# Kernel tuning notes

Hardware: AMD Instinct MI355X
Metric: run time of the kernel (lower is better)

Reference implementation:

```python
import math
import jax, jax.numpy as jnp
import numpy as np

B, S, E = 4, 2048, 1024

def setup_inputs() -> dict:
    key = jax.random.key(0)
    k1, k2, k3 = jax.random.split(key, 3)
    X = jax.random.normal(k1, (B, S, E), dtype=jnp.float32)
    # nn.Linear(E, 3E): weight [3E, E], bias [3E]; scale weights for sane softmax
    W = jax.random.normal(k2, (3 * E, E), dtype=jnp.float32) * (1.0 / math.sqrt(E))
    b = jax.random.normal(k3, (3 * E,), dtype=jnp.float32) * 0.01
    return {"X": X, "W": W, "b": b}

def reference(X, W, b):
    E_ = X.shape[-1]
    # fused QKV projection: X @ W^T + b -> [B, S, 3E]
    qkv = jnp.einsum('bse,fe->bsf', X, W) + b
    q, k, v = jnp.split(qkv, 3, axis=-1)
    scores = jnp.einsum('bqe,bke->bqk', q, k) / math.sqrt(E_)
    attention_weight = jax.nn.softmax(scores, axis=-1)  # [B, S, S]
    output = jnp.einsum('bqk,bke->bqe', attention_weight, v)
    return (output, attention_weight)
```

## Files before the change

### kernel.cpp

```cpp
#include <hip/hip_runtime.h>
#include <math.h>

typedef __bf16 bf16;
typedef __bf16 bf16x4 __attribute__((ext_vector_type(4)));
typedef __bf16 bf16x8 __attribute__((ext_vector_type(8)));
typedef float f32x4 __attribute__((ext_vector_type(4)));

#define MODE_QKV    0
#define MODE_SCORES 1
#define MODE_PV     2

__device__ inline void gload_lds16(const bf16* g, bf16* l) {
    __builtin_amdgcn_global_load_lds(
        (const __attribute__((address_space(1))) void*)g,
        (__attribute__((address_space(3))) void*)l, 16, 0, 0);
}

#define DSR(dst, base, imm)                                                 \
    asm volatile("ds_read_b128 %0, %1 offset:%2"                            \
        : "=v"(dst)                                                         \
        : "v"((const __attribute__((address_space(3))) bf16*)(base)),       \
          "i"(imm))

#define MF(i, j) acc[i][j] = __builtin_amdgcn_mfma_f32_16x16x32_bf16(       \
    af[i], bq[j], acc[i][j], 0, 0, 0);

template <int MODE, int NT>
__global__ __launch_bounds__(256, 2) void mfma_nt(
    const bf16* __restrict__ A, const bf16* __restrict__ B,
    const float* __restrict__ bias, void* __restrict__ Cv,
    int lda, int ldb, int ldc,
    long sA, long sB, long sC, float alpha)
{
    A += (long)blockIdx.z * sA;
    B += (long)blockIdx.z * sB;

    __shared__ bf16 As[3 * 8192] __attribute__((aligned(16)));
    __shared__ bf16 Bs[3 * 4096] __attribute__((aligned(16)));

    const int t  = threadIdx.x;
    const int m0 = blockIdx.y * 256;
    const int n0 = blockIdx.x * 128;

    const int lane = t & 63;
    const int wave = t >> 6;
    const int wr   = (wave >> 1) * 128;
    const int wc   = (wave & 1) * 64;
    const int fr   = lane & 15;
    const int kq8  = lane >> 4;

    const bf16* gA0; const bf16* gA1; const bf16* gA2; const bf16* gA3;
    const bf16* gB0; const bf16* gB1;
    {
        const int c0 = t,        r0 = c0 >> 2, h0 = ((c0 & 3) ^ ((r0 >> 1) & 3)) * 8;
        const int c1 = t + 256,  r1 = c1 >> 2, h1 = ((c1 & 3) ^ ((r1 >> 1) & 3)) * 8;
        const int c2 = t + 512,  r2 = c2 >> 2, h2 = ((c2 & 3) ^ ((r2 >> 1) & 3)) * 8;
        const int c3 = t + 768,  r3 = c3 >> 2, h3 = ((c3 & 3) ^ ((r3 >> 1) & 3)) * 8;
        gA0 = A + (long)(m0 + r0) * lda + h0;
        gA1 = A + (long)(m0 + r1) * lda + h1;
        gA2 = A + (long)(m0 + r2) * lda + h2;
        gA3 = A + (long)(m0 + r3) * lda + h3;
        gB0 = B + (long)(n0 + r0) * ldb + h0;
        gB1 = B + (long)(n0 + r1) * ldb + h1;
    }

    const int swz = kq8 ^ ((fr >> 1) & 3);
    const bf16* pA = As + (wr + fr) * 32 + swz * 8;
    const bf16* pB = Bs + (wc + fr) * 32 + swz * 8;

    f32x4 acc[8][4] = {};
    bf16x8 af[8], bq[4];
    int kofs = 64;

#define STAGE6(SS, ko)                                                      \
    gload_lds16(gA0 + (ko), &As[(SS) * 8192 + t * 8]);                      \
    gload_lds16(gA1 + (ko), &As[(SS) * 8192 + (t + 256) * 8]);              \
    gload_lds16(gA2 + (ko), &As[(SS) * 8192 + (t + 512) * 8]);              \
    gload_lds16(gA3 + (ko), &As[(SS) * 8192 + (t + 768) * 8]);              \
    gload_lds16(gB0 + (ko), &Bs[(SS) * 4096 + t * 8]);                      \
    gload_lds16(gB1 + (ko), &Bs[(SS) * 4096 + (t + 256) * 8]);

#define TB(CS, STG) do {                                                    \
    if constexpr ((STG) == 1) {                                             \
        constexpr int SS = ((CS) + 2) % 3;                                  \
        STAGE6(SS, kofs);                                                   \
        kofs += 32;                                                         \
    }                                                                       \
    DSR(af[0], pA, (CS) * 16384 + 0);                                       \
    DSR(af[1], pA, (CS) * 16384 + 1024);                                    \
    DSR(af[2], pA, (CS) * 16384 + 2048);                                    \
    DSR(af[3], pA, (CS) * 16384 + 3072);                                    \
    DSR(bq[0], pB, (CS) * 8192 + 0);                                        \
    DSR(bq[1], pB, (CS) * 8192 + 1024);                                     \
    DSR(bq[2], pB, (CS) * 8192 + 2048);                                     \
    DSR(bq[3], pB, (CS) * 8192 + 3072);                                     \
    DSR(af[4], pA, (CS) * 16384 + 4096);                                    \
    DSR(af[5], pA, (CS) * 16384 + 5120);                                    \
    DSR(af[6], pA, (CS) * 16384 + 6144);                                    \
    DSR(af[7], pA, (CS) * 16384 + 7168);                                    \
    asm volatile("s_waitcnt lgkmcnt(6)" ::: "memory");                      \
    __builtin_amdgcn_sched_barrier(0);                                      \
    __builtin_amdgcn_s_setprio(1);                                          \
    MF(0,0) MF(0,1) MF(1,0) MF(1,1) MF(2,0) MF(2,1) MF(3,0) MF(3,1)         \
    asm volatile("s_waitcnt lgkmcnt(4)" ::: "memory");                      \
    __builtin_amdgcn_sched_barrier(0);                                      \
    MF(0,2) MF(0,3) MF(1,2) MF(1,3) MF(2,2) MF(2,3) MF(3,2) MF(3,3)         \
    asm volatile("s_waitcnt lgkmcnt(0)" ::: "memory");                      \
    __builtin_amdgcn_sched_barrier(0);                                      \
    MF(4,0) MF(4,1) MF(5,0) MF(5,1) MF(6,0) MF(6,1) MF(7,0) MF(7,1)         \
    MF(4,2) MF(4,3) MF(5,2) MF(5,3) MF(6,2) MF(6,3) MF(7,2) MF(7,3)         \
    __builtin_amdgcn_s_setprio(0);                                          \
    if constexpr ((STG) == 1)                                               \
        asm volatile("s_waitcnt vmcnt(6)" ::: "memory");                    \
    else if constexpr ((STG) == 0)                                          \
        asm volatile("s_waitcnt vmcnt(0)" ::: "memory");                    \
    if constexpr ((STG) != 2) __builtin_amdgcn_s_barrier();                 \
} while (0)

    STAGE6(0, 0);
    STAGE6(1, 32);
    asm volatile("s_waitcnt vmcnt(6)" ::: "memory");
    __builtin_amdgcn_s_barrier();

    static_assert(NT % 3 != 0, "peel pattern assumes NT%3 in {1,2}");
    if constexpr (NT % 3 == 2) {
        TB(0, 1); TB(1, 1);
        for (int g = 0; g < (NT - 5) / 3; ++g) { TB(2, 1); TB(0, 1); TB(1, 1); }
        TB(2, 1); TB(0, 0); TB(1, 2);
    } else {
        TB(0, 1);
        for (int g = 0; g < (NT - 4) / 3; ++g) { TB(1, 1); TB(2, 1); TB(0, 1); }
        TB(1, 1); TB(2, 0); TB(0, 2);
    }
#undef TB
#undef STAGE6

    const int r4 = (lane >> 4) * 4;
    if constexpr (MODE == MODE_PV) {
        float* C = (float*)Cv + (long)blockIdx.z * sC;
#pragma unroll
        for (int j = 0; j < 4; j++) {
            const int col = n0 + wc + j * 16 + fr;
#pragma unroll
            for (int i = 0; i < 8; i++)
#pragma unroll
                for (int r = 0; r < 4; r++) {
                    const long row = m0 + wr + i * 16 + r4 + r;
                    C[row * ldc + col] = acc[i][j][r];
                }
        }
    } else {
        bf16* C = (bf16*)Cv + (long)blockIdx.z * sC;
#pragma unroll
        for (int j = 0; j < 4; j++) {
            const int col = n0 + wc + j * 16 + fr;
            const float bv = (MODE == MODE_QKV) ? bias[col] : 0.f;
#pragma unroll
            for (int i = 0; i < 8; i++)
#pragma unroll
                for (int r = 0; r < 4; r++) {
                    const long row = m0 + wr + i * 16 + r4 + r;
                    float v = acc[i][j][r];
                    if constexpr (MODE == MODE_QKV)
                        C[row * ldc + col] = (bf16)(v + bv);
                    else
                        C[row * ldc + col] = (bf16)__expf(alpha * v);
                }
        }
    }
}

__global__ __launch_bounds__(256) void f32_to_bf16(
    const float* __restrict__ in, bf16* __restrict__ out, long n)
{
    long i = ((long)blockIdx.x * 256 + threadIdx.x) * 4;
    if (i < n) {
        float4 v = *(const float4*)(in + i);
        bf16x4 o = { (bf16)v.x, (bf16)v.y, (bf16)v.z, (bf16)v.w };
        *(bf16x4*)(out + i) = o;
    }
}

__global__ __launch_bounds__(256) void transpose_v(
    const bf16* __restrict__ V, bf16* __restrict__ Vt)
{
    __shared__ bf16 tile[32][33];
    const bf16* Vb  = V  + (long)blockIdx.z * 2048 * 3072;
    bf16*       Vtb = Vt + (long)blockIdx.z * 1024 * 2048;
    const int s0 = blockIdx.x * 32, e0 = blockIdx.y * 32;
    const int tx = threadIdx.x & 31, ty = threadIdx.x >> 5;
#pragma unroll
    for (int i = 0; i < 32; i += 8)
        tile[ty + i][tx] = Vb[(long)(s0 + ty + i) * 3072 + e0 + tx];
    __syncthreads();
#pragma unroll
    for (int i = 0; i < 32; i += 8)
        Vtb[(long)(e0 + ty + i) * 2048 + s0 + tx] = tile[tx][ty + i];
}

__global__ __launch_bounds__(256) void norm_rows(
    bf16* __restrict__ Pu, float* __restrict__ out1)
{
    bf16* p  = Pu   + (long)blockIdx.x * 2048;
    float* o = out1 + (long)blockIdx.x * 2048;
    const int t = threadIdx.x;
    bf16x8 v = *(const bf16x8*)(p + t * 8);
    float f[8];
    float s = 0.f;
#pragma unroll
    for (int k = 0; k < 8; k++) { f[k] = (float)v[k]; s += f[k]; }
#pragma unroll
    for (int off = 32; off > 0; off >>= 1) s += __shfl_xor(s, off);
    __shared__ float red[4];
    const int wid = t >> 6, lane = t & 63;
    if (lane == 0) red[wid] = s;
    __syncthreads();
    s = red[0] + red[1] + red[2] + red[3];
    const float inv = 1.0f / s;
    float4 a, b;
    a.x = f[0] * inv; a.y = f[1] * inv; a.z = f[2] * inv; a.w = f[3] * inv;
    b.x = f[4] * inv; b.y = f[5] * inv; b.z = f[6] * inv; b.w = f[7] * inv;
    *(float4*)(o + t * 8)     = a;
    *(float4*)(o + t * 8 + 4) = b;
    bf16x8 w;
#pragma unroll
    for (int k = 0; k < 8; k++) w[k] = (bf16)(f[k] * inv);
    *(bf16x8*)(p + t * 8) = w;
}

extern "C" void kernel_launch(void* const* d_in, const int* in_sizes, int n_in,
                              void* d_out, int out_size, void* d_ws, size_t ws_size,
                              hipStream_t stream)
{
    const int B = 4, S = 2048, E = 1024;
    const float* X    = (const float*)d_in[0];
    const float* W    = (const float*)d_in[1];
    const float* bias = (const float*)d_in[2];

    float* out0 = (float*)d_out;
    float* out1 = out0 + (long)B * S * E;

    char* ws = (char*)d_ws;
    bf16* qkvb = (bf16*)(ws);
    bf16* Vt   = (bf16*)(ws + 50331648);
    bf16* Pu   = (bf16*)(ws + 67108864);
    bf16* Xb   = (bf16*)(ws + 67108864);
    bf16* Wb   = (bf16*)(ws + 83886080);

    f32_to_bf16<<<(long)B * S * E / 1024, 256, 0, stream>>>(X, Xb, (long)B * S * E);
    f32_to_bf16<<<(long)3 * E * E / 1024, 256, 0, stream>>>(W, Wb, (long)3 * E * E);

    mfma_nt<MODE_QKV, 32><<<dim3(3 * E / 128, B * S / 256, 1), 256, 0, stream>>>(
        Xb, Wb, bias, qkvb, E, E, 3 * E, 0, 0, 0, 1.0f);

    transpose_v<<<dim3(S / 32, E / 32, B), 256, 0, stream>>>(qkvb + 2 * E, Vt);

    mfma_nt<MODE_SCORES, 32><<<dim3(S / 128, S / 256, B), 256, 0, stream>>>(
        qkvb, qkvb + E, nullptr, Pu, 3 * E, 3 * E, S,
        (long)S * 3 * E, (long)S * 3 * E, (long)S * S, 0.03125f);

    norm_rows<<<B * S, 256, 0, stream>>>(Pu, out1);

    mfma_nt<MODE_PV, 64><<<dim3(E / 128, S / 256, B), 256, 0, stream>>>(
        Pu, Vt, nullptr, out0, S, S, E,
        (long)S * S, (long)E * S, (long)S * E, 1.0f);
}
```

Measured before the change: 304.1 us.

## Split-K the PV GEMM with atomics and use a 2-slot LDS ring for QKV

The PV GEMM is split into two K halves across blockIdx.z, doubling the grid. Partial results are accumulated into a zeroed output via atomic float adds, which needs a memset first. Separately, the QKV projection switches to a 2-stage LDS ring with full vmcnt waits, freeing shared memory at the cost of less load/compute overlap. The PV grid was only 128 blocks, so the split aims to fill more CUs, but it adds atomic traffic and an extra memset pass over the output.

```diff
diff --git a/kernel.cpp b/kernel.cpp
--- a/kernel.cpp
+++ b/kernel.cpp
@@ -25,18 +25,23 @@
 #define MF(i, j) acc[i][j] = __builtin_amdgcn_mfma_f32_16x16x32_bf16(       \
     af[i], bq[j], acc[i][j], 0, 0, 0);
 
-template <int MODE, int NT>
+template <int MODE, int NT, int RING>
 __global__ __launch_bounds__(256, 2) void mfma_nt(
     const bf16* __restrict__ A, const bf16* __restrict__ B,
     const float* __restrict__ bias, void* __restrict__ Cv,
     int lda, int ldb, int ldc,
     long sA, long sB, long sC, float alpha)
 {
-    A += (long)blockIdx.z * sA;
-    B += (long)blockIdx.z * sB;
-
-    __shared__ bf16 As[3 * 8192] __attribute__((aligned(16)));
-    __shared__ bf16 Bs[3 * 4096] __attribute__((aligned(16)));
+    constexpr bool SPLIT = (MODE == MODE_PV);
+
+    const int bz    = blockIdx.z;
+    const int batch = SPLIT ? (bz >> 1) : bz;
+    const int koff  = SPLIT ? (bz & 1) * (NT * 32) : 0;
+    A += (long)batch * sA + koff;
+    B += (long)batch * sB + koff;
+
+    __shared__ bf16 As[RING * 8192] __attribute__((aligned(16)));
+    __shared__ bf16 Bs[RING * 4096] __attribute__((aligned(16)));
 
     const int t  = threadIdx.x;
     const int m0 = blockIdx.y * 256;
@@ -70,7 +75,7 @@
 
     f32x4 acc[8][4] = {};
     bf16x8 af[8], bq[4];
-    int kofs = 64;
+    int kofs;
 
 #define STAGE6(SS, ko)                                                      \
     gload_lds16(gA0 + (ko), &As[(SS) * 8192 + t * 8]);                      \
@@ -82,7 +87,7 @@
 
 #define TB(CS, STG) do {                                                    \
     if constexpr ((STG) == 1) {                                             \
-        constexpr int SS = ((CS) + 2) % 3;                                  \
+        constexpr int SS = ((CS) + RING - 1) % RING;                        \
         STAGE6(SS, kofs);                                                   \
         kofs += 32;                                                         \
     }                                                                       \
@@ -110,34 +115,49 @@
     MF(4,0) MF(4,1) MF(5,0) MF(5,1) MF(6,0) MF(6,1) MF(7,0) MF(7,1)         \
     MF(4,2) MF(4,3) MF(5,2) MF(5,3) MF(6,2) MF(6,3) MF(7,2) MF(7,3)         \
     __builtin_amdgcn_s_setprio(0);                                          \
-    if constexpr ((STG) == 1)                                               \
-        asm volatile("s_waitcnt vmcnt(6)" ::: "memory");                    \
-    else if constexpr ((STG) == 0)                                          \
+    if constexpr ((STG) == 1) {                                             \
+        if constexpr (RING == 3)                                            \
+            asm volatile("s_waitcnt vmcnt(6)" ::: "memory");                \
+        else                                                                \
+            asm volatile("s_waitcnt vmcnt(0)" ::: "memory");                \
+    } else if constexpr ((STG) == 0)                                        \
         asm volatile("s_waitcnt vmcnt(0)" ::: "memory");                    \
     if constexpr ((STG) != 2) __builtin_amdgcn_s_barrier();                 \
 } while (0)
 
-    STAGE6(0, 0);
-    STAGE6(1, 32);
-    asm volatile("s_waitcnt vmcnt(6)" ::: "memory");
-    __builtin_amdgcn_s_barrier();
-
-    static_assert(NT % 3 != 0, "peel pattern assumes NT%3 in {1,2}");
-    if constexpr (NT % 3 == 2) {
-        TB(0, 1); TB(1, 1);
-        for (int g = 0; g < (NT - 5) / 3; ++g) { TB(2, 1); TB(0, 1); TB(1, 1); }
-        TB(2, 1); TB(0, 0); TB(1, 2);
+    if constexpr (RING == 3) {
+        STAGE6(0, 0);
+        STAGE6(1, 32);
+        kofs = 64;
+        asm volatile("s_waitcnt vmcnt(6)" ::: "memory");
+        __builtin_amdgcn_s_barrier();
+
+        static_assert(NT % 3 != 0, "peel pattern assumes NT%3 in {1,2}");
+        if constexpr (NT % 3 == 2) {
+            TB(0, 1); TB(1, 1);
+            for (int g = 0; g < (NT - 5) / 3; ++g) { TB(2, 1); TB(0, 1); TB(1, 1); }
+            TB(2, 1); TB(0, 0); TB(1, 2);
+        } else {
+            TB(0, 1);
+            for (int g = 0; g < (NT - 4) / 3; ++g) { TB(1, 1); TB(2, 1); TB(0, 1); }
+            TB(1, 1); TB(2, 0); TB(0, 2);
+        }
     } else {
-        TB(0, 1);
-        for (int g = 0; g < (NT - 4) / 3; ++g) { TB(1, 1); TB(2, 1); TB(0, 1); }
-        TB(1, 1); TB(2, 0); TB(0, 2);
+        STAGE6(0, 0);
+        kofs = 32;
+        asm volatile("s_waitcnt vmcnt(0)" ::: "memory");
+        __builtin_amdgcn_s_barrier();
+
+        static_assert(NT % 2 == 0, "2-slot peel assumes even NT");
+        for (int g = 0; g < NT / 2 - 1; ++g) { TB(0, 1); TB(1, 1); }
+        TB(0, 1); TB(1, 2);
     }
 #undef TB
 #undef STAGE6
 
     const int r4 = (lane >> 4) * 4;
     if constexpr (MODE == MODE_PV) {
-        float* C = (float*)Cv + (long)blockIdx.z * sC;
+        float* C = (float*)Cv + (long)batch * sC;
 #pragma unroll
         for (int j = 0; j < 4; j++) {
             const int col = n0 + wc + j * 16 + fr;
@@ -146,11 +166,11 @@
 #pragma unroll
                 for (int r = 0; r < 4; r++) {
                     const long row = m0 + wr + i * 16 + r4 + r;
-                    C[row * ldc + col] = acc[i][j][r];
+                    unsafeAtomicAdd(&C[row * ldc + col], acc[i][j][r]);
                 }
         }
     } else {
-        bf16* C = (bf16*)Cv + (long)blockIdx.z * sC;
+        bf16* C = (bf16*)Cv + (long)batch * sC;
 #pragma unroll
         for (int j = 0; j < 4; j++) {
             const int col = n0 + wc + j * 16 + fr;
@@ -250,18 +270,19 @@
     f32_to_bf16<<<(long)B * S * E / 1024, 256, 0, stream>>>(X, Xb, (long)B * S * E);
     f32_to_bf16<<<(long)3 * E * E / 1024, 256, 0, stream>>>(W, Wb, (long)3 * E * E);
 
-    mfma_nt<MODE_QKV, 32><<<dim3(3 * E / 128, B * S / 256, 1), 256, 0, stream>>>(
+    mfma_nt<MODE_QKV, 32, 2><<<dim3(3 * E / 128, B * S / 256, 1), 256, 0, stream>>>(
         Xb, Wb, bias, qkvb, E, E, 3 * E, 0, 0, 0, 1.0f);
 
     transpose_v<<<dim3(S / 32, E / 32, B), 256, 0, stream>>>(qkvb + 2 * E, Vt);
 
-    mfma_nt<MODE_SCORES, 32><<<dim3(S / 128, S / 256, B), 256, 0, stream>>>(
+    mfma_nt<MODE_SCORES, 32, 3><<<dim3(S / 128, S / 256, B), 256, 0, stream>>>(
         qkvb, qkvb + E, nullptr, Pu, 3 * E, 3 * E, S,
         (long)S * 3 * E, (long)S * 3 * E, (long)S * S, 0.03125f);
 
     norm_rows<<<B * S, 256, 0, stream>>>(Pu, out1);
 
-    mfma_nt<MODE_PV, 64><<<dim3(E / 128, S / 256, B), 256, 0, stream>>>(
+    hipMemsetAsync(out0, 0, (size_t)B * S * E * sizeof(float), stream);
+    mfma_nt<MODE_PV, 32, 3><<<dim3(E / 128, S / 256, 2 * B), 256, 0, stream>>>(
         Pu, Vt, nullptr, out0, S, S, E,
         (long)S * S, (long)E * S, (long)S * E, 1.0f);
 }
```

New measurement: 359.7 us. 1.18x slower.

## Prefetch next K-tile's A/B fragments from LDS during second MFMA half

Applied to the files above, without the earlier changes.

Restructures the GEMM main loop so the lower A fragments and all B fragments for the next K-step are read from LDS right after the barrier, while the upper-half MFMAs of the current step run. Fragments are double-buffered in registers, and the global-to-LDS stage is issued mid-iteration. The loop peel is rewritten for NT of 32 or 64 only. This aims to hide LDS read latency behind MFMA work, at the cost of more VGPRs under launch_bounds(256,2), which risks spills or lower occupancy.

```diff
diff --git a/kernel.cpp b/kernel.cpp
--- a/kernel.cpp
+++ b/kernel.cpp
@@ -21,9 +21,6 @@
         : "=v"(dst)                                                         \
         : "v"((const __attribute__((address_space(3))) bf16*)(base)),       \
           "i"(imm))
-
-#define MF(i, j) acc[i][j] = __builtin_amdgcn_mfma_f32_16x16x32_bf16(       \
-    af[i], bq[j], acc[i][j], 0, 0, 0);
 
 template <int MODE, int NT>
 __global__ __launch_bounds__(256, 2) void mfma_nt(
@@ -69,8 +66,10 @@
     const bf16* pB = Bs + (wc + fr) * 32 + swz * 8;
 
     f32x4 acc[8][4] = {};
-    bf16x8 af[8], bq[4];
-    int kofs = 64;
+    bf16x8 afhi[4];
+    bf16x8 alo[2][4];
+    bf16x8 bqq[2][4];
+    int kofs;
 
 #define STAGE6(SS, ko)                                                      \
     gload_lds16(gA0 + (ko), &As[(SS) * 8192 + t * 8]);                      \
@@ -80,60 +79,84 @@
     gload_lds16(gB0 + (ko), &Bs[(SS) * 4096 + t * 8]);                      \
     gload_lds16(gB1 + (ko), &Bs[(SS) * 4096 + (t + 256) * 8]);
 
-#define TB(CS, STG) do {                                                    \
-    if constexpr ((STG) == 1) {                                             \
-        constexpr int SS = ((CS) + 2) % 3;                                  \
-        STAGE6(SS, kofs);                                                   \
-        kofs += 32;                                                         \
-    }                                                                       \
-    DSR(af[0], pA, (CS) * 16384 + 0);                                       \
-    DSR(af[1], pA, (CS) * 16384 + 1024);                                    \
-    DSR(af[2], pA, (CS) * 16384 + 2048);                                    \
-    DSR(af[3], pA, (CS) * 16384 + 3072);                                    \
-    DSR(bq[0], pB, (CS) * 8192 + 0);                                        \
-    DSR(bq[1], pB, (CS) * 8192 + 1024);                                     \
-    DSR(bq[2], pB, (CS) * 8192 + 2048);                                     \
-    DSR(bq[3], pB, (CS) * 8192 + 3072);                                     \
-    DSR(af[4], pA, (CS) * 16384 + 4096);                                    \
-    DSR(af[5], pA, (CS) * 16384 + 5120);                                    \
-    DSR(af[6], pA, (CS) * 16384 + 6144);                                    \
-    DSR(af[7], pA, (CS) * 16384 + 7168);                                    \
-    asm volatile("s_waitcnt lgkmcnt(6)" ::: "memory");                      \
+#define MFU(i, j, P) acc[i][j] = __builtin_amdgcn_mfma_f32_16x16x32_bf16(   \
+    alo[P][i], bqq[P][j], acc[i][j], 0, 0, 0);
+#define MFL(i, j, P) acc[4 + i][j] = __builtin_amdgcn_mfma_f32_16x16x32_bf16(\
+    afhi[i], bqq[P][j], acc[4 + i][j], 0, 0, 0);
+
+#define TBP(C, P, STG) do {                                                 \
+    DSR(afhi[0], pA, (C) * 16384 + 4096);                                   \
+    DSR(afhi[1], pA, (C) * 16384 + 5120);                                   \
+    DSR(afhi[2], pA, (C) * 16384 + 6144);                                   \
+    DSR(afhi[3], pA, (C) * 16384 + 7168);                                   \
+    asm volatile("s_waitcnt lgkmcnt(4)" ::: "memory");                      \
     __builtin_amdgcn_sched_barrier(0);                                      \
     __builtin_amdgcn_s_setprio(1);                                          \
-    MF(0,0) MF(0,1) MF(1,0) MF(1,1) MF(2,0) MF(2,1) MF(3,0) MF(3,1)         \
-    asm volatile("s_waitcnt lgkmcnt(4)" ::: "memory");                      \
-    __builtin_amdgcn_sched_barrier(0);                                      \
-    MF(0,2) MF(0,3) MF(1,2) MF(1,3) MF(2,2) MF(2,3) MF(3,2) MF(3,3)         \
+    MFU(0,0,P) MFU(0,1,P) MFU(1,0,P) MFU(1,1,P)                             \
+    MFU(2,0,P) MFU(2,1,P) MFU(3,0,P) MFU(3,1,P)                             \
+    MFU(0,2,P) MFU(0,3,P) MFU(1,2,P) MFU(1,3,P)                             \
+    MFU(2,2,P) MFU(2,3,P) MFU(3,2,P) MFU(3,3,P)                             \
+    __builtin_amdgcn_s_setprio(0);                                          \
+    if constexpr ((STG) == 1) { STAGE6(((C) + 2) % 3, kofs); kofs += 32; }  \
     asm volatile("s_waitcnt lgkmcnt(0)" ::: "memory");                      \
     __builtin_amdgcn_sched_barrier(0);                                      \
-    MF(4,0) MF(4,1) MF(5,0) MF(5,1) MF(6,0) MF(6,1) MF(7,0) MF(7,1)         \
-    MF(4,2) MF(4,3) MF(5,2) MF(5,3) MF(6,2) MF(6,3) MF(7,2) MF(7,3)         \
-    __builtin_amdgcn_s_setprio(0);                                          \
     if constexpr ((STG) == 1)                                               \
         asm volatile("s_waitcnt vmcnt(6)" ::: "memory");                    \
     else if constexpr ((STG) == 0)                                          \
         asm volatile("s_waitcnt vmcnt(0)" ::: "memory");                    \
-    if constexpr ((STG) != 2) __builtin_amdgcn_s_barrier();                 \
+    if constexpr ((STG) != 2) {                                             \
+        __builtin_amdgcn_s_barrier();                                       \
+        DSR(alo[(P)^1][0], pA, (((C)+1)%3) * 16384 + 0);                    \
+        DSR(alo[(P)^1][1], pA, (((C)+1)%3) * 16384 + 1024);                 \
+        DSR(alo[(P)^1][2], pA, (((C)+1)%3) * 16384 + 2048);                 \
+        DSR(alo[(P)^1][3], pA, (((C)+1)%3) * 16384 + 3072);                 \
+        DSR(bqq[(P)^1][0], pB, (((C)+1)%3) * 8192 + 0);                     \
+        DSR(bqq[(P)^1][1], pB, (((C)+1)%3) * 8192 + 1024);                  \
+        DSR(bqq[(P)^1][2], pB, (((C)+1)%3) * 8192 + 2048);                  \
+        DSR(bqq[(P)^1][3], pB, (((C)+1)%3) * 8192 + 3072);                  \
+        __builtin_amdgcn_sched_barrier(0);                                  \
+    }                                                                       \
+    __builtin_amdgcn_s_setprio(1);                                          \
+    MFL(0,0,P) MFL(0,1,P) MFL(1,0,P) MFL(1,1,P)                             \
+    MFL(2,0,P) MFL(2,1,P) MFL(3,0,P) MFL(3,1,P)                             \
+    MFL(0,2,P) MFL(0,3,P) MFL(1,2,P) MFL(1,3,P)                             \
+    MFL(2,2,P) MFL(2,3,P) MFL(3,2,P) MFL(3,3,P)                             \
+    __builtin_amdgcn_s_setprio(0);                                          \
 } while (0)
 
     STAGE6(0, 0);
     STAGE6(1, 32);
+    kofs = 64;
     asm volatile("s_waitcnt vmcnt(6)" ::: "memory");
     __builtin_amdgcn_s_barrier();
-
-    static_assert(NT % 3 != 0, "peel pattern assumes NT%3 in {1,2}");
-    if constexpr (NT % 3 == 2) {
-        TB(0, 1); TB(1, 1);
-        for (int g = 0; g < (NT - 5) / 3; ++g) { TB(2, 1); TB(0, 1); TB(1, 1); }
-        TB(2, 1); TB(0, 0); TB(1, 2);
+    DSR(alo[0][0], pA, 0);
+    DSR(alo[0][1], pA, 1024);
+    DSR(alo[0][2], pA, 2048);
+    DSR(alo[0][3], pA, 3072);
+    DSR(bqq[0][0], pB, 0);
+    DSR(bqq[0][1], pB, 1024);
+    DSR(bqq[0][2], pB, 2048);
+    DSR(bqq[0][3], pB, 3072);
+
+    static_assert(NT == 32 || NT == 64, "peel assumes NT in {32,64}");
+    if constexpr (NT == 32) {
+        for (int g = 0; g < 5; ++g) {
+            TBP(0,0,1); TBP(1,1,1); TBP(2,0,1);
+            TBP(0,1,1); TBP(1,0,1); TBP(2,1,1);
+        }
+        TBP(0,0,0); TBP(1,1,2);
     } else {
-        TB(0, 1);
-        for (int g = 0; g < (NT - 4) / 3; ++g) { TB(1, 1); TB(2, 1); TB(0, 1); }
-        TB(1, 1); TB(2, 0); TB(0, 2);
-    }
-#undef TB
+        for (int g = 0; g < 10; ++g) {
+            TBP(0,0,1); TBP(1,1,1); TBP(2,0,1);
+            TBP(0,1,1); TBP(1,0,1); TBP(2,1,1);
+        }
+        TBP(0,0,1); TBP(1,1,1);
+        TBP(2,0,0); TBP(0,1,2);
+    }
+#undef TBP
 #undef STAGE6
+#undef MFU
+#undef MFL
 
     const int r4 = (lane >> 4) * 4;
     if constexpr (MODE == MODE_PV) {
```

Measured after the change: 305.1 us. About the same (+0.3%).

## Use 8 waves per block with smaller per-wave tiles in MFMA GEMM

Applied to the files above, without the earlier changes.

Doubles the block to 512 threads (8 waves) while keeping the 256x128 block tile, so each wave computes a 64x64 sub-tile instead of 128x64. Per-thread accumulators and fragment registers halve, and each thread issues 3 global-to-LDS loads per stage instead of 6. The prefetch for the next stage moves into the middle of the MFMA sequence to overlap with compute. The aim is more waves to hide latency and lower register pressure, at the cost of more LDS reads per MFMA and more barrier participants.

```diff
diff --git a/kernel.cpp b/kernel.cpp
--- a/kernel.cpp
+++ b/kernel.cpp
@@ -26,7 +26,7 @@
     af[i], bq[j], acc[i][j], 0, 0, 0);
 
 template <int MODE, int NT>
-__global__ __launch_bounds__(256, 2) void mfma_nt(
+__global__ __launch_bounds__(512) void mfma_nt(
     const bf16* __restrict__ A, const bf16* __restrict__ B,
     const float* __restrict__ bias, void* __restrict__ Cv,
     int lda, int ldb, int ldc,
@@ -44,82 +44,66 @@
 
     const int lane = t & 63;
     const int wave = t >> 6;
-    const int wr   = (wave >> 1) * 128;
+    const int wr   = (wave >> 1) * 64;
     const int wc   = (wave & 1) * 64;
     const int fr   = lane & 15;
     const int kq8  = lane >> 4;
 
-    const bf16* gA0; const bf16* gA1; const bf16* gA2; const bf16* gA3;
-    const bf16* gB0; const bf16* gB1;
+    const bf16* gA0; const bf16* gA1; const bf16* gB0;
     {
         const int c0 = t,        r0 = c0 >> 2, h0 = ((c0 & 3) ^ ((r0 >> 1) & 3)) * 8;
-        const int c1 = t + 256,  r1 = c1 >> 2, h1 = ((c1 & 3) ^ ((r1 >> 1) & 3)) * 8;
-        const int c2 = t + 512,  r2 = c2 >> 2, h2 = ((c2 & 3) ^ ((r2 >> 1) & 3)) * 8;
-        const int c3 = t + 768,  r3 = c3 >> 2, h3 = ((c3 & 3) ^ ((r3 >> 1) & 3)) * 8;
+        const int c1 = t + 512,  r1 = c1 >> 2, h1 = ((c1 & 3) ^ ((r1 >> 1) & 3)) * 8;
         gA0 = A + (long)(m0 + r0) * lda + h0;
         gA1 = A + (long)(m0 + r1) * lda + h1;
-        gA2 = A + (long)(m0 + r2) * lda + h2;
-        gA3 = A + (long)(m0 + r3) * lda + h3;
         gB0 = B + (long)(n0 + r0) * ldb + h0;
-        gB1 = B + (long)(n0 + r1) * ldb + h1;
     }
 
     const int swz = kq8 ^ ((fr >> 1) & 3);
     const bf16* pA = As + (wr + fr) * 32 + swz * 8;
     const bf16* pB = Bs + (wc + fr) * 32 + swz * 8;
 
-    f32x4 acc[8][4] = {};
-    bf16x8 af[8], bq[4];
-    int kofs = 64;
-
-#define STAGE6(SS, ko)                                                      \
+    f32x4 acc[4][4] = {};
+    bf16x8 af[4], bq[4];
+    int kofs;
+
+#define STAGE3(SS, ko)                                                      \
     gload_lds16(gA0 + (ko), &As[(SS) * 8192 + t * 8]);                      \
-    gload_lds16(gA1 + (ko), &As[(SS) * 8192 + (t + 256) * 8]);              \
-    gload_lds16(gA2 + (ko), &As[(SS) * 8192 + (t + 512) * 8]);              \
-    gload_lds16(gA3 + (ko), &As[(SS) * 8192 + (t + 768) * 8]);              \
-    gload_lds16(gB0 + (ko), &Bs[(SS) * 4096 + t * 8]);                      \
-    gload_lds16(gB1 + (ko), &Bs[(SS) * 4096 + (t + 256) * 8]);
+    gload_lds16(gA1 + (ko), &As[(SS) * 8192 + (t + 512) * 8]);              \
+    gload_lds16(gB0 + (ko), &Bs[(SS) * 4096 + t * 8]);
 
 #define TB(CS, STG) do {                                                    \
-    if constexpr ((STG) == 1) {                                             \
-        constexpr int SS = ((CS) + 2) % 3;                                  \
-        STAGE6(SS, kofs);                                                   \
-        kofs += 32;                                                         \
-    }                                                                       \
     DSR(af[0], pA, (CS) * 16384 + 0);                                       \
     DSR(af[1], pA, (CS) * 16384 + 1024);                                    \
-    DSR(af[2], pA, (CS) * 16384 + 2048);                                    \
-    DSR(af[3], pA, (CS) * 16384 + 3072);                                    \
     DSR(bq[0], pB, (CS) * 8192 + 0);                                        \
     DSR(bq[1], pB, (CS) * 8192 + 1024);                                     \
     DSR(bq[2], pB, (CS) * 8192 + 2048);                                     \
     DSR(bq[3], pB, (CS) * 8192 + 3072);                                     \
-    DSR(af[4], pA, (CS) * 16384 + 4096);                                    \
-    DSR(af[5], pA, (CS) * 16384 + 5120);                                    \
-    DSR(af[6], pA, (CS) * 16384 + 6144);                                    \
-    DSR(af[7], pA, (CS) * 16384 + 7168);                                    \
-    asm volatile("s_waitcnt lgkmcnt(6)" ::: "memory");                      \
+    DSR(af[2], pA, (CS) * 16384 + 2048);                                    \
+    DSR(af[3], pA, (CS) * 16384 + 3072);                                    \
+    asm volatile("s_waitcnt lgkmcnt(2)" ::: "memory");                      \
     __builtin_amdgcn_sched_barrier(0);                                      \
     __builtin_amdgcn_s_setprio(1);                                          \
-    MF(0,0) MF(0,1) MF(1,0) MF(1,1) MF(2,0) MF(2,1) MF(3,0) MF(3,1)         \
-    asm volatile("s_waitcnt lgkmcnt(4)" ::: "memory");                      \
-    __builtin_amdgcn_sched_barrier(0);                                      \
-    MF(0,2) MF(0,3) MF(1,2) MF(1,3) MF(2,2) MF(2,3) MF(3,2) MF(3,3)         \
+    MF(0,0) MF(0,1) MF(1,0) MF(1,1)                                         \
+    MF(0,2) MF(0,3) MF(1,2) MF(1,3)                                         \
+    __builtin_amdgcn_s_setprio(0);                                          \
+    if constexpr ((STG) == 1) { STAGE3(((CS) + 2) % 3, kofs); kofs += 32; } \
     asm volatile("s_waitcnt lgkmcnt(0)" ::: "memory");                      \
     __builtin_amdgcn_sched_barrier(0);                                      \
-    MF(4,0) MF(4,1) MF(5,0) MF(5,1) MF(6,0) MF(6,1) MF(7,0) MF(7,1)         \
-    MF(4,2) MF(4,3) MF(5,2) MF(5,3) MF(6,2) MF(6,3) MF(7,2) MF(7,3)         \
+    __builtin_amdgcn_s_setprio(1);                                          \
+    MF(2,0) MF(2,1) MF(3,0) MF(3,1)                                         \
+    MF(2,2) MF(2,3) MF(3,2) MF(3,3)                                         \
     __builtin_amdgcn_s_setprio(0);                                          \
     if constexpr ((STG) == 1)                                               \
-        asm volatile("s_waitcnt vmcnt(6)" ::: "memory");                    \
+        asm volatile("s_waitcnt vmcnt(3)" ::: "memory");                    \
     else if constexpr ((STG) == 0)                                          \
         asm volatile("s_waitcnt vmcnt(0)" ::: "memory");                    \
     if constexpr ((STG) != 2) __builtin_amdgcn_s_barrier();                 \
 } while (0)
 
-    STAGE6(0, 0);
-    STAGE6(1, 32);
-    asm volatile("s_waitcnt vmcnt(6)" ::: "memory");
+    STAGE3(0, 0);
+    STAGE3(1, 32);
+    kofs = 64;
+    asm volatile("s_waitcnt vmcnt(3)" ::: "memory");
     __builtin_amdgcn_s_barrier();
 
     static_assert(NT % 3 != 0, "peel pattern assumes NT%3 in {1,2}");
@@ -133,7 +117,7 @@
         TB(1, 1); TB(2, 0); TB(0, 2);
     }
 #undef TB
-#undef STAGE6
+#undef STAGE3
 
     const int r4 = (lane >> 4) * 4;
     if constexpr (MODE == MODE_PV) {
@@ -142,7 +126,7 @@
         for (int j = 0; j < 4; j++) {
             const int col = n0 + wc + j * 16 + fr;
 #pragma unroll
-            for (int i = 0; i < 8; i++)
+            for (int i = 0; i < 4; i++)
 #pragma unroll
                 for (int r = 0; r < 4; r++) {
                     const long row = m0 + wr + i * 16 + r4 + r;
@@ -156,7 +140,7 @@
             const int col = n0 + wc + j * 16 + fr;
             const float bv = (MODE == MODE_QKV) ? bias[col] : 0.f;
 #pragma unroll
-            for (int i = 0; i < 8; i++)
+            for (int i = 0; i < 4; i++)
 #pragma unroll
                 for (int r = 0; r < 4; r++) {
                     const long row = m0 + wr + i * 16 + r4 + r;
@@ -250,18 +234,18 @@
     f32_to_bf16<<<(long)B * S * E / 1024, 256, 0, stream>>>(X, Xb, (long)B * S * E);
     f32_to_bf16<<<(long)3 * E * E / 1024, 256, 0, stream>>>(W, Wb, (long)3 * E * E);
 
-    mfma_nt<MODE_QKV, 32><<<dim3(3 * E / 128, B * S / 256, 1), 256, 0, stream>>>(
+    mfma_nt<MODE_QKV, 32><<<dim3(3 * E / 128, B * S / 256, 1), 512, 0, stream>>>(
         Xb, Wb, bias, qkvb, E, E, 3 * E, 0, 0, 0, 1.0f);
 
     transpose_v<<<dim3(S / 32, E / 32, B), 256, 0, stream>>>(qkvb + 2 * E, Vt);
 
-    mfma_nt<MODE_SCORES, 32><<<dim3(S / 128, S / 256, B), 256, 0, stream>>>(
+    mfma_nt<MODE_SCORES, 32><<<dim3(S / 128, S / 256, B), 512, 0, stream>>>(
         qkvb, qkvb + E, nullptr, Pu, 3 * E, 3 * E, S,
         (long)S * 3 * E, (long)S * 3 * E, (long)S * S, 0.03125f);
 
     norm_rows<<<B * S, 256, 0, stream>>>(Pu, out1);
 
-    mfma_nt<MODE_PV, 64><<<dim3(E / 128, S / 256, B), 256, 0, stream>>>(
+    mfma_nt<MODE_PV, 64><<<dim3(E / 128, S / 256, B), 512, 0, stream>>>(
         Pu, Vt, nullptr, out0, S, S, E,
         (long)S * S, (long)E * S, (long)S * E, 1.0f);
 }
```

Measured after the change: 296.7 us. 1.03x faster.
